# Kernel optimization log

Hardware: AMD Instinct MI355X
Metric: run time of the kernel (lower is better)

The kernel has to match this reference:

```python
import jax, jax.numpy as jnp
import numpy as np

DIM = 1024

def setup_inputs() -> dict:
    key = jax.random.key(0)
    k1, k2, k3, k4 = jax.random.split(key, 4)
    x = jax.random.normal(k1, (4, 4096, DIM), dtype=jnp.float32)
    A = jax.random.normal(k2, (DIM, DIM), dtype=jnp.float32) * 0.01
    B_w = jax.random.normal(k3, (DIM, DIM), dtype=jnp.float32) * (1.0 / np.sqrt(DIM))
    C_w = jax.random.normal(k4, (DIM, DIM), dtype=jnp.float32) * (1.0 / np.sqrt(DIM))
    D = jnp.ones((DIM,), dtype=jnp.float32)
    return {"x": x, "A": A, "B_w": B_w, "C_w": C_w, "D": D}

def reference(x, A, B_w, C_w, D):
    # x: [B, L, Dm]; recurrence: h_t = tanh(h_{t-1} @ A.T + x_t @ B_w.T)
    #                 y_t = h_t @ C_w.T + D * x_t
    Bsz, L, Dm = x.shape
    # Precompute the input projection for all steps at once (one big GEMM).
    bx = jnp.einsum('bld,ed->ble', x, B_w)  # [B, L, Dm]

    def step(h, inputs):
        bx_t, x_t = inputs
        h = jnp.tanh(h @ A.T + bx_t)
        y = h @ C_w.T + D * x_t
        return h, y

    h0 = jnp.zeros((Bsz, Dm), dtype=x.dtype)
    # scan over time axis: move L to leading dim
    _, ys = jax.lax.scan(step, h0, (jnp.swapaxes(bx, 0, 1), jnp.swapaxes(x, 0, 1)))
    return jnp.swapaxes(ys, 0, 1)  # [B, L, Dm]
```

## Files before the change

kernel.cpp:

```cpp
#include <hip/hip_runtime.h>
#include <math.h>

#define DM   1024
#define BSZ  4
#define LSEQ 4096
#define GPB  32
#define RPW  32
#define TPB  512
#define SEGC 64
#define SSP  68
#define HSW2 1088
#define CRS  1092

typedef unsigned long long u64;

__global__ __launch_bounds__(256) void bx_gemm_kernel(
    const float* __restrict__ X, const float* __restrict__ Bw,
    float* __restrict__ out)
{
    __shared__ float xs[16][68];
    __shared__ float bs[16][68];
    const int bm = blockIdx.x, bn = blockIdx.y;
    const int t  = threadIdx.x;
    const int tx = t & 15, ty = t >> 4;
    const int ml = t >> 2;
    const int kq = (t & 3) * 4;
    const float* xg = X  + (size_t)(bm * 64 + ml) * DM + kq;
    const float* bg = Bw + (size_t)(bn * 64 + ml) * DM + kq;
    float acc[4][4] = {};
    for (int k0 = 0; k0 < DM; k0 += 16) {
        float4 xv = *(const float4*)(xg + k0);
        float4 bv = *(const float4*)(bg + k0);
        __syncthreads();
        xs[kq+0][ml] = xv.x; xs[kq+1][ml] = xv.y; xs[kq+2][ml] = xv.z; xs[kq+3][ml] = xv.w;
        bs[kq+0][ml] = bv.x; bs[kq+1][ml] = bv.y; bs[kq+2][ml] = bv.z; bs[kq+3][ml] = bv.w;
        __syncthreads();
        #pragma unroll
        for (int kk = 0; kk < 16; ++kk) {
            float a[4], c[4];
            #pragma unroll
            for (int i = 0; i < 4; ++i) a[i] = xs[kk][ty*4+i];
            #pragma unroll
            for (int j = 0; j < 4; ++j) c[j] = bs[kk][tx*4+j];
            #pragma unroll
            for (int i = 0; i < 4; ++i)
                #pragma unroll
                for (int j = 0; j < 4; ++j)
                    acc[i][j] += a[i] * c[j];
        }
    }
    #pragma unroll
    for (int i = 0; i < 4; ++i) {
        float4 v = make_float4(acc[i][0], acc[i][1], acc[i][2], acc[i][3]);
        *(float4*)(out + (size_t)(bm*64 + ty*4 + i)*DM + bn*64 + tx*4) = v;
    }
}

__device__ __forceinline__ u64 poll_word(u64* fast, u64* safe, unsigned tag,
                                         u64 v, int& fastok)
{
    if ((unsigned)(v >> 32) == tag) return v;
    if (fastok) {
        #pragma unroll 1
        for (int i = 0; i < 16; ++i) {
            v = __hip_atomic_fetch_add(fast, 0ULL, __ATOMIC_RELAXED,
                                       __HIP_MEMORY_SCOPE_WORKGROUP);
            if ((unsigned)(v >> 32) == tag) return v;
        }
    }
    int spins = 0;
    do {
        v = __hip_atomic_load(safe, __ATOMIC_RELAXED, __HIP_MEMORY_SCOPE_AGENT);
    } while ((unsigned)(v >> 32) != tag && ++spins < (1 << 20));
    if (fastok) {
        u64 f = __hip_atomic_fetch_add(fast, 0ULL, __ATOMIC_RELAXED,
                                       __HIP_MEMORY_SCOPE_WORKGROUP);
        if ((unsigned)(f >> 32) != tag) fastok = 0;
    }
    return v;
}

__global__ __launch_bounds__(TPB, 1) void scan_kernel(
    const float* __restrict__ A, const float* __restrict__ Cw,
    const float* __restrict__ Dv, const float* __restrict__ X,
    float* __restrict__ Y, u64* hfast, u64* hsafe)
{
    const int r = blockIdx.x & 7;
    if (r >= BSZ) return;
    const int b  = r;
    const int gw = blockIdx.x >> 3;
    const int r0 = gw * RPW;

    extern __shared__ float lds[];
    float* cs  = lds;
    float* hs0 = lds + RPW * CRS;
    const int t   = threadIdx.x;
    const int row = t >> 4;
    const int seg = t & 15;
    const bool lead = (seg == 0);

    float ra[SEGC];
    {
        const float* Ap = A + (size_t)(r0 + row) * DM + seg * SEGC;
        #pragma unroll
        for (int u = 0; u < SEGC / 4; ++u) {
            float4 v = *(const float4*)(Ap + u*4);
            ra[u*4+0]=v.x; ra[u*4+1]=v.y; ra[u*4+2]=v.z; ra[u*4+3]=v.w;
        }
    }
    for (int i = 0; i < 16; ++i) {
        int idx = i * TPB + t;
        int rr  = idx >> 8;
        int c4  = idx & 255;
        float4 v = *(const float4*)(Cw + (size_t)(r0 + rr) * DM + c4 * 4);
        *(float4*)(cs + rr * CRS + (c4 >> 4) * SSP + (c4 & 15) * 4) = v;
    }
    const float dv = Dv[r0 + row];
    __syncthreads();

    const int c0 = t, c1 = t + 512;
    const int s0 = (c0 >> 6) * SSP + (c0 & 63);
    const int s1 = (c1 >> 6) * SSP + (c1 & 63);
    int fastok = 1;

    u64 v0 = __hip_atomic_load(hsafe + (size_t)b * DM + c0, __ATOMIC_RELAXED, __HIP_MEMORY_SCOPE_AGENT);
    u64 v1 = __hip_atomic_load(hsafe + (size_t)b * DM + c1, __ATOMIC_RELAXED, __HIP_MEMORY_SCOPE_AGENT);
    float bxv = 0.f;
    float xv  = 0.f;
    if (lead) bxv = Y[(size_t)b*LSEQ*DM + r0 + row];

    for (int k = 0; k <= LSEQ; ++k) {
        const unsigned tag = (unsigned)k;
        const size_t slot = (size_t)(k & 1) * BSZ * DM + (size_t)b * DM;
        int dummy = 0;
        int& fo = (k == 0) ? dummy : fastok;

        v0 = poll_word(hfast + slot + c0, hsafe + slot + c0, tag, v0, fo);
        v1 = poll_word(hfast + slot + c1, hsafe + slot + c1, tag, v1, fo);

        float* hsk = hs0 + (k & 1) * HSW2;
        hsk[s0] = __uint_as_float((unsigned)v0);
        hsk[s1] = __uint_as_float((unsigned)v1);
        __syncthreads();

        const float4* h4p = (const float4*)(hsk + seg * SSP);
        float xv_next = xv;
        if (k < LSEQ) {
            float accA = 0.f;
            #pragma unroll
            for (int u = 0; u < SEGC / 4; ++u) {
                float4 h4 = h4p[u];
                accA += ra[u*4+0]*h4.x + ra[u*4+1]*h4.y + ra[u*4+2]*h4.z + ra[u*4+3]*h4.w;
            }
            accA += __shfl_xor(accA, 1);
            accA += __shfl_xor(accA, 2);
            accA += __shfl_xor(accA, 4);
            accA += __shfl_xor(accA, 8);
            const size_t nslot = (size_t)((k+1) & 1) * BSZ * DM + (size_t)b * DM;
            if (lead) {
                float hv = tanhf(accA + bxv);
                u64 pk = ((u64)(unsigned)(k + 1) << 32) | (u64)__float_as_uint(hv);
                __hip_atomic_store(hfast + nslot + r0 + row, pk,
                                   __ATOMIC_RELAXED, __HIP_MEMORY_SCOPE_WORKGROUP);
                __hip_atomic_store(hsafe + nslot + r0 + row, pk,
                                   __ATOMIC_RELAXED, __HIP_MEMORY_SCOPE_AGENT);
            }
            if (fastok) {
                v0 = __hip_atomic_fetch_add(hfast + nslot + c0, 0ULL,
                                            __ATOMIC_RELAXED, __HIP_MEMORY_SCOPE_WORKGROUP);
                v1 = __hip_atomic_fetch_add(hfast + nslot + c1, 0ULL,
                                            __ATOMIC_RELAXED, __HIP_MEMORY_SCOPE_WORKGROUP);
            } else {
                v0 = __hip_atomic_load(hsafe + nslot + c0, __ATOMIC_RELAXED, __HIP_MEMORY_SCOPE_AGENT);
                v1 = __hip_atomic_load(hsafe + nslot + c1, __ATOMIC_RELAXED, __HIP_MEMORY_SCOPE_AGENT);
            }
            if (lead) {
                xv_next = X[(size_t)b*LSEQ*DM + (size_t)k*DM + r0 + row];
                if (k + 1 < LSEQ)
                    bxv = Y[(size_t)b*LSEQ*DM + (size_t)(k+1)*DM + r0 + row];
            }
        }

        if (k > 0) {
            float accC = 0.f;
            const float4* c4p = (const float4*)(cs + row * CRS + seg * SSP);
            #pragma unroll
            for (int u = 0; u < SEGC / 4; ++u) {
                float4 c4 = c4p[u];
                float4 h4 = h4p[u];
                accC += c4.x*h4.x + c4.y*h4.y + c4.z*h4.z + c4.w*h4.w;
            }
            accC += __shfl_xor(accC, 1);
            accC += __shfl_xor(accC, 2);
            accC += __shfl_xor(accC, 4);
            accC += __shfl_xor(accC, 8);
            if (lead) {
                const size_t yoff = (size_t)b*LSEQ*DM + (size_t)(k-1)*DM + r0 + row;
                Y[yoff] = accC + dv * xv;
            }
        }
        xv = xv_next;
    }
}

extern "C" void kernel_launch(void* const* d_in, const int* in_sizes, int n_in,
                              void* d_out, int out_size, void* d_ws, size_t ws_size,
                              hipStream_t stream)
{
    const float* X  = (const float*)d_in[0];
    const float* A  = (const float*)d_in[1];
    const float* Bw = (const float*)d_in[2];
    const float* Cw = (const float*)d_in[3];
    const float* Dv = (const float*)d_in[4];
    float* Y    = (float*)d_out;
    u64* hfast  = (u64*)d_ws;
    u64* hsafe  = hfast + (size_t)2 * BSZ * DM;

    hipMemsetAsync(d_ws, 0, (size_t)4 * BSZ * DM * sizeof(u64), stream);

    dim3 g1((BSZ * LSEQ) / 64, DM / 64);
    bx_gemm_kernel<<<g1, 256, 0, stream>>>(X, Bw, Y);
    const size_t lds_bytes = (size_t)(RPW * CRS + 2 * HSW2) * sizeof(float);
    scan_kernel<<<256, TPB, lds_bytes, stream>>>(A, Cw, Dv, X, Y, hfast, hsafe);
}
```

Baseline: 10.70 ms.

## Keep C_w in registers, fuse A and C dot products, use fast tanh

Loads each thread's C_w slice into registers instead of staging it in shared memory, and computes the A and C dot products in one loop over the shared h vector. Replaces tanhf with an exp-based approximation and changes the launch bound to allow two blocks per CU. This removes the LDS reads of C each step but doubles register use and puts the output dot product before the recurrence's critical path. The exp-based tanh can overflow to NaN for large inputs.

```diff
diff --git a/kernel.cpp b/kernel.cpp
--- a/kernel.cpp
+++ b/kernel.cpp
@@ -10,7 +10,6 @@
 #define SEGC 64
 #define SSP  68
 #define HSW2 1088
-#define CRS  1092
 
 typedef unsigned long long u64;
 
@@ -80,7 +79,13 @@
     return v;
 }
 
-__global__ __launch_bounds__(TPB, 1) void scan_kernel(
+__device__ __forceinline__ float fast_tanh(float x)
+{
+    float e = __expf(2.0f * x);
+    return (e - 1.0f) / (e + 1.0f);
+}
+
+__global__ __launch_bounds__(TPB, 2) void scan_kernel(
     const float* __restrict__ A, const float* __restrict__ Cw,
     const float* __restrict__ Dv, const float* __restrict__ X,
     float* __restrict__ Y, u64* hfast, u64* hsafe)
@@ -91,32 +96,25 @@
     const int gw = blockIdx.x >> 3;
     const int r0 = gw * RPW;
 
-    extern __shared__ float lds[];
-    float* cs  = lds;
-    float* hs0 = lds + RPW * CRS;
+    __shared__ float hs0[2 * HSW2];
     const int t   = threadIdx.x;
     const int row = t >> 4;
     const int seg = t & 15;
     const bool lead = (seg == 0);
 
-    float ra[SEGC];
+    float ra[SEGC], rc[SEGC];
     {
-        const float* Ap = A + (size_t)(r0 + row) * DM + seg * SEGC;
+        const float* Ap = A  + (size_t)(r0 + row) * DM + seg * SEGC;
+        const float* Cp = Cw + (size_t)(r0 + row) * DM + seg * SEGC;
         #pragma unroll
         for (int u = 0; u < SEGC / 4; ++u) {
             float4 v = *(const float4*)(Ap + u*4);
             ra[u*4+0]=v.x; ra[u*4+1]=v.y; ra[u*4+2]=v.z; ra[u*4+3]=v.w;
-        }
-    }
-    for (int i = 0; i < 16; ++i) {
-        int idx = i * TPB + t;
-        int rr  = idx >> 8;
-        int c4  = idx & 255;
-        float4 v = *(const float4*)(Cw + (size_t)(r0 + rr) * DM + c4 * 4);
-        *(float4*)(cs + rr * CRS + (c4 >> 4) * SSP + (c4 & 15) * 4) = v;
+            float4 w = *(const float4*)(Cp + u*4);
+            rc[u*4+0]=w.x; rc[u*4+1]=w.y; rc[u*4+2]=w.z; rc[u*4+3]=w.w;
+        }
     }
     const float dv = Dv[r0 + row];
-    __syncthreads();
 
     const int c0 = t, c1 = t + 512;
     const int s0 = (c0 >> 6) * SSP + (c0 & 63);
@@ -143,22 +141,26 @@
         hsk[s1] = __uint_as_float((unsigned)v1);
         __syncthreads();
 
-        const float4* h4p = (const float4*)(hsk + seg * SSP);
-        float xv_next = xv;
-        if (k < LSEQ) {
-            float accA = 0.f;
+        float accA = 0.f, accC = 0.f;
+        {
+            const float4* h4p = (const float4*)(hsk + seg * SSP);
             #pragma unroll
             for (int u = 0; u < SEGC / 4; ++u) {
                 float4 h4 = h4p[u];
                 accA += ra[u*4+0]*h4.x + ra[u*4+1]*h4.y + ra[u*4+2]*h4.z + ra[u*4+3]*h4.w;
-            }
+                accC += rc[u*4+0]*h4.x + rc[u*4+1]*h4.y + rc[u*4+2]*h4.z + rc[u*4+3]*h4.w;
+            }
+        }
+
+        float xv_next = xv;
+        if (k < LSEQ) {
             accA += __shfl_xor(accA, 1);
             accA += __shfl_xor(accA, 2);
             accA += __shfl_xor(accA, 4);
             accA += __shfl_xor(accA, 8);
             const size_t nslot = (size_t)((k+1) & 1) * BSZ * DM + (size_t)b * DM;
             if (lead) {
-                float hv = tanhf(accA + bxv);
+                float hv = fast_tanh(accA + bxv);
                 u64 pk = ((u64)(unsigned)(k + 1) << 32) | (u64)__float_as_uint(hv);
                 __hip_atomic_store(hfast + nslot + r0 + row, pk,
                                    __ATOMIC_RELAXED, __HIP_MEMORY_SCOPE_WORKGROUP);
@@ -182,14 +184,6 @@
         }
 
         if (k > 0) {
-            float accC = 0.f;
-            const float4* c4p = (const float4*)(cs + row * CRS + seg * SSP);
-            #pragma unroll
-            for (int u = 0; u < SEGC / 4; ++u) {
-                float4 c4 = c4p[u];
-                float4 h4 = h4p[u];
-                accC += c4.x*h4.x + c4.y*h4.y + c4.z*h4.z + c4.w*h4.w;
-            }
             accC += __shfl_xor(accC, 1);
             accC += __shfl_xor(accC, 2);
             accC += __shfl_xor(accC, 4);
@@ -220,6 +214,5 @@
 
     dim3 g1((BSZ * LSEQ) / 64, DM / 64);
     bx_gemm_kernel<<<g1, 256, 0, stream>>>(X, Bw, Y);
-    const size_t lds_bytes = (size_t)(RPW * CRS + 2 * HSW2) * sizeof(float);
-    scan_kernel<<<256, TPB, lds_bytes, stream>>>(A, Cw, Dv, X, Y, hfast, hsafe);
-}
+    scan_kernel<<<256, TPB, 0, stream>>>(A, Cw, Dv, X, Y, hfast, hsafe);
+}
```

Result: slower. 11.42 ms (+6.7%).
